# Performance work log

Measured on AMD Instinct MI355X. Metric: run time of the kernel, lower is better.

## Reference

```python
import jax, jax.numpy as jnp
import numpy as np

B, L, D = 4, 2048, 256
DI, DS, DCONV, DTR, K = 512, 16, 4, 16, 3  # d_inner, d_state, mamba conv, dt_rank, outer conv kernel
PAD = 1 * (K - 1)  # dilation*(kernel_size-1)
ALPHA = 0.5


def setup_inputs() -> dict:
    key = jax.random.key(0)
    ks = jax.random.split(key, 14)
    s = lambda k, shape, scale: jax.random.normal(k, shape, dtype=jnp.float32) * scale
    inp = {
        "x": s(ks[0], (B, L, D), 1.0),
        "ln_w": jnp.ones((D,), jnp.float32),
        "ln_b": jnp.zeros((D,), jnp.float32),
        "conv_w": s(ks[1], (D, D, K), 0.05),          # outer Conv1d weight (out,in,k)
        "conv_b": s(ks[2], (D,), 0.02),
        "in_proj_w": s(ks[3], (2 * DI, D), 0.05),      # Mamba in_proj (no bias)
        "conv1d_w": s(ks[4], (DI, 1, DCONV), 0.3),     # depthwise causal conv
        "conv1d_b": s(ks[5], (DI,), 0.02),
        "x_proj_w": s(ks[6], (DTR + 2 * DS, DI), 0.05),
        "dt_proj_w": s(ks[7], (DI, DTR), 0.1),
        "dt_proj_b": s(ks[8], (DI,), 0.1),
        "A_log": jnp.log(jnp.broadcast_to(jnp.arange(1, DS + 1, dtype=jnp.float32), (DI, DS))),
        "D_param": jnp.ones((DI,), jnp.float32),
        "out_proj_w": s(ks[9], (D, DI), 0.05),
    }
    return inp


def _layernorm(h, w, b):
    mu = jnp.mean(h, axis=-1, keepdims=True)
    var = jnp.mean(jnp.square(h - mu), axis=-1, keepdims=True)
    return (h - mu) * jax.lax.rsqrt(var + 1e-5) * w + b


def _causal_conv(h_ncl, w, pad, groups):
    # h_ncl: (B, C, L); left-pad only -> output length L (matches pad-then-slice in torch)
    return jax.lax.conv_general_dilated(
        h_ncl, w, window_strides=(1,), padding=[(pad, 0)],
        dimension_numbers=("NCH", "OIH", "NCH"), feature_group_count=groups)


def _mamba(h, in_proj_w, conv1d_w, conv1d_b, x_proj_w, dt_proj_w, dt_proj_b, A_log, D_param, out_proj_w):
    xz = jnp.einsum("bld,ed->ble", h, in_proj_w)          # (B,L,2*DI)
    xin, z = jnp.split(xz, 2, axis=-1)
    xc = _causal_conv(xin.transpose(0, 2, 1), conv1d_w, DCONV - 1, DI)
    xc = jax.nn.silu(xc + conv1d_b[None, :, None]).transpose(0, 2, 1)   # (B,L,DI)
    x_dbl = jnp.einsum("bld,ed->ble", xc, x_proj_w)
    dt, Bm, Cm = jnp.split(x_dbl, [DTR, DTR + DS], axis=-1)
    delta = jax.nn.softplus(jnp.einsum("blr,dr->bld", dt, dt_proj_w) + dt_proj_b)  # (B,L,DI)
    A = -jnp.exp(A_log)                                     # (DI,DS)
    dA = jnp.exp(delta[..., None] * A)                      # (B,L,DI,DS)
    dBx = delta[..., None] * Bm[:, :, None, :] * xc[..., None]

    def step(hst, t):
        dA_t, dBx_t, C_t = t
        hst = dA_t * hst + dBx_t                            # (B,DI,DS)
        y = jnp.einsum("bds,bs->bd", hst, C_t)
        return hst, y

    h0 = jnp.zeros((h.shape[0], DI, DS), h.dtype)
    _, ys = jax.lax.scan(step, h0, (dA.transpose(1, 0, 2, 3), dBx.transpose(1, 0, 2, 3), Cm.transpose(1, 0, 2)))
    y = ys.transpose(1, 0, 2) + xc * D_param                # (B,L,DI)
    y = y * jax.nn.silu(z)
    return jnp.einsum("ble,de->bld", y, out_proj_w)


def reference(x, ln_w, ln_b, conv_w, conv_b, in_proj_w, conv1d_w, conv1d_b,
              x_proj_w, dt_proj_w, dt_proj_b, A_log, D_param, out_proj_w):
    h = _layernorm(x, ln_w, ln_b)
    # conv branch: pad left, conv, GELU (exact erf, as torch nn.GELU)
    hc = _causal_conv(h.transpose(0, 2, 1), conv_w, PAD, 1) + conv_b[None, :, None]
    h_conv = jax.nn.gelu(hc, approximate=False).transpose(0, 2, 1)
    h_mamba = _mamba(h, in_proj_w, conv1d_w, conv1d_b, x_proj_w, dt_proj_w,
                     dt_proj_b, A_log, D_param, out_proj_w)
    h_out = ALPHA * h_mamba + (1.0 - ALPHA) * h_conv
    return x + h_out
```

## Files before the change

kernel.cpp:

```cpp
#include <hip/hip_runtime.h>
#include <math.h>

#define BBATCH 4
#define LSEQ   2048
#define DMODEL 256
#define DINNER 512
#define DSTATE 16
#define DTRANK 16
#define MROWS  (BBATCH * LSEQ)
#define NCHUNK 64
#define LCHUNK (LSEQ / NCHUNK)

typedef unsigned short u16;
typedef __attribute__((ext_vector_type(8))) short bf16x8;
typedef __attribute__((ext_vector_type(4))) float f32x4;

#define OFF_HBF    ((size_t)0)
#define OFF_HCONV  ((size_t)1048576)
#define OFF_XIN    ((size_t)3145728)
#define OFF_Z      ((size_t)7340032)
#define OFF_XC     ((size_t)11534336)
#define OFF_DELTA  ((size_t)15728640)
#define OFF_XDBL   ((size_t)19922944)
#define OFF_YBF    ((size_t)20316160)
#define OFF_AAGG   ((size_t)22413312)
#define OFF_BAGG   ((size_t)24510464)
#define OFF_HINIT  OFF_AAGG
#define OFF_WTINBF ((size_t)26607616)
#define OFF_WTCVBF ((size_t)26738688)
#define OFF_WTOUTBF ((size_t)26836992)
#define OFF_WTX    ((size_t)26902528)
#define OFF_WTDT   ((size_t)26927104)

__device__ __forceinline__ float silu_f(float v) {
  return v / (1.0f + __expf(-v));
}
__device__ __forceinline__ u16 f2bf(float f) {
  unsigned u = __float_as_uint(f);
  return (u16)((u + 0x7FFFu + ((u >> 16) & 1u)) >> 16);
}
__device__ __forceinline__ float bf2f(u16 v) {
  return __uint_as_float(((unsigned)v) << 16);
}

__global__ __launch_bounds__(256) void k_repack(
    const float* __restrict__ inw, const float* __restrict__ convw,
    const float* __restrict__ xw, const float* __restrict__ dtw,
    const float* __restrict__ ow, float* __restrict__ ws) {
  int idx = blockIdx.x * 256 + threadIdx.x;
  u16* win  = (u16*)(ws + OFF_WTINBF);
  u16* wcv  = (u16*)(ws + OFF_WTCVBF);
  u16* wout = (u16*)(ws + OFF_WTOUTBF);
  float* wx  = ws + OFF_WTX;
  float* wdt = ws + OFF_WTDT;
  if (idx < 262144) {
    win[idx] = f2bf(inw[idx]);
    return;
  }
  int i2 = idx - 262144;
  if (i2 < 196608) {
    int o = i2 / 768, r = i2 - o * 768;
    int kk = r >> 8, i = r & 255;
    wcv[i2] = f2bf(convw[(o * 256 + i) * 3 + kk]);
    return;
  }
  int i3 = i2 - 196608;
  if (i3 < 131072) {
    wout[i3] = f2bf(ow[i3]);
    return;
  }
  int i4 = i3 - 131072;
  if (i4 < 24576) {
    int k = i4 / 48, n = i4 - k * 48;
    wx[i4] = xw[n * 512 + k];
    return;
  }
  int i5 = i4 - 24576;
  if (i5 < 8192) {
    int r = i5 >> 9, n = i5 & 511;
    wdt[i5] = dtw[n * 16 + r];
  }
}

__global__ __launch_bounds__(256) void k_layernorm(
    const float* __restrict__ x, const float* __restrict__ w,
    const float* __restrict__ b, u16* __restrict__ hb) {
  int wave = threadIdx.x >> 6;
  int lane = threadIdx.x & 63;
  int row  = blockIdx.x * 4 + wave;
  const float4* xr = reinterpret_cast<const float4*>(x + (size_t)row * 256);
  float4 v = xr[lane];
  float s  = v.x + v.y + v.z + v.w;
  float sq = v.x*v.x + v.y*v.y + v.z*v.z + v.w*v.w;
  #pragma unroll
  for (int o = 32; o >= 1; o >>= 1) { s += __shfl_xor(s, o); sq += __shfl_xor(sq, o); }
  float mu  = s * (1.0f / 256.0f);
  float var = sq * (1.0f / 256.0f) - mu * mu;
  float rs  = rsqrtf(var + 1e-5f);
  float4 wv = reinterpret_cast<const float4*>(w)[lane];
  float4 bv = reinterpret_cast<const float4*>(b)[lane];
  ushort4 o4;
  o4.x = f2bf((v.x - mu) * rs * wv.x + bv.x);
  o4.y = f2bf((v.y - mu) * rs * wv.y + bv.y);
  o4.z = f2bf((v.z - mu) * rs * wv.z + bv.z);
  o4.w = f2bf((v.w - mu) * rs * wv.w + bv.w);
  reinterpret_cast<ushort4*>(hb + (size_t)row * 256)[lane] = o4;
}


__global__ __launch_bounds__(256) void k_bgemm_inproj(
    const u16* __restrict__ Abf, const u16* __restrict__ Bbf,
    u16* __restrict__ xin, u16* __restrict__ z) {
  __shared__ __align__(16) u16 As[64 * 72];
  __shared__ __align__(16) u16 Bs[128 * 72];
  int tid = threadIdx.x;
  int m0 = blockIdx.x * 64, n0 = blockIdx.y * 128;
  int lane = tid & 63, wid = tid >> 6;
  int wc = wid * 32;
  int l15 = lane & 15, lk = (lane >> 4) * 8;
  int r0 = tid >> 3, kc = (tid & 7) * 8;
  f32x4 acc[4][2] = {};
  for (int k0 = 0; k0 < 256; k0 += 64) {
    *(bf16x8*)&As[r0 * 72 + kc] =
        *(const bf16x8*)&Abf[(size_t)(m0 + r0) * 256 + k0 + kc];
    *(bf16x8*)&As[(r0 + 32) * 72 + kc] =
        *(const bf16x8*)&Abf[(size_t)(m0 + r0 + 32) * 256 + k0 + kc];
    #pragma unroll
    for (int rr = 0; rr < 4; ++rr)
      *(bf16x8*)&Bs[(r0 + rr * 32) * 72 + kc] =
          *(const bf16x8*)&Bbf[(size_t)(n0 + r0 + rr * 32) * 256 + k0 + kc];
    __syncthreads();
    #pragma unroll
    for (int kk = 0; kk < 64; kk += 32) {
      bf16x8 b0 = *(const bf16x8*)&Bs[(wc + l15) * 72 + kk + lk];
      bf16x8 b1 = *(const bf16x8*)&Bs[(wc + 16 + l15) * 72 + kk + lk];
      #pragma unroll
      for (int q = 0; q < 4; ++q) {
        bf16x8 a = *(const bf16x8*)&As[(q * 16 + l15) * 72 + kk + lk];
        acc[q][0] = __builtin_amdgcn_mfma_f32_16x16x32_bf16(a, b0, acc[q][0], 0, 0, 0);
        acc[q][1] = __builtin_amdgcn_mfma_f32_16x16x32_bf16(a, b1, acc[q][1], 0, 0, 0);
      }
    }
    __syncthreads();
  }
  u16* dst = (blockIdx.y < 4) ? xin : z;
  int nb = n0 & 511;
  int rsub = (lane >> 4) * 4;
  #pragma unroll
  for (int q = 0; q < 4; ++q)
    #pragma unroll
    for (int ni = 0; ni < 2; ++ni) {
      int gc = nb + wc + ni * 16 + l15;
      #pragma unroll
      for (int r = 0; r < 4; ++r)
        dst[(size_t)(m0 + q * 16 + rsub + r) * 512 + gc] = f2bf(acc[q][ni][r]);
    }
}

__global__ __launch_bounds__(256) void k_bgemm_conv(
    const u16* __restrict__ hbf, const u16* __restrict__ Bbf,
    const float* __restrict__ cb, float* __restrict__ hconv) {
  __shared__ __align__(16) u16 As[64 * 72];
  __shared__ __align__(16) u16 Bs[64 * 72];
  int tid = threadIdx.x;
  int m0 = blockIdx.x * 64, n0 = blockIdx.y * 64;
  int bidx = m0 >> 11, t0 = m0 & 2047;
  int lane = tid & 63, wid = tid >> 6;
  int wr = (wid >> 1) * 32, wc = (wid & 1) * 32;
  int l15 = lane & 15, lk = (lane >> 4) * 8;
  int r0 = tid >> 3, kc = (tid & 7) * 8;
  f32x4 acc[2][2] = {};
  for (int k0 = 0; k0 < 768; k0 += 64) {
    int kkc = k0 >> 8;
    int i0  = (k0 & 255) + kc;
    int t1  = t0 + r0 - 2 + kkc;
    bf16x8 av0 = {0, 0, 0, 0, 0, 0, 0, 0};
    if (t1 >= 0)
      av0 = *(const bf16x8*)&hbf[(size_t)((bidx << 11) + t1) * 256 + i0];
    bf16x8 av1 =
        *(const bf16x8*)&hbf[(size_t)((bidx << 11) + t1 + 32) * 256 + i0];
    *(bf16x8*)&As[r0 * 72 + kc] = av0;
    *(bf16x8*)&As[(r0 + 32) * 72 + kc] = av1;
    *(bf16x8*)&Bs[r0 * 72 + kc] =
        *(const bf16x8*)&Bbf[(size_t)(n0 + r0) * 768 + k0 + kc];
    *(bf16x8*)&Bs[(r0 + 32) * 72 + kc] =
        *(const bf16x8*)&Bbf[(size_t)(n0 + r0 + 32) * 768 + k0 + kc];
    __syncthreads();
    #pragma unroll
    for (int kk = 0; kk < 64; kk += 32) {
      bf16x8 a0 = *(const bf16x8*)&As[(wr + l15) * 72 + kk + lk];
      bf16x8 a1 = *(const bf16x8*)&As[(wr + 16 + l15) * 72 + kk + lk];
      bf16x8 b0 = *(const bf16x8*)&Bs[(wc + l15) * 72 + kk + lk];
      bf16x8 b1 = *(const bf16x8*)&Bs[(wc + 16 + l15) * 72 + kk + lk];
      acc[0][0] = __builtin_amdgcn_mfma_f32_16x16x32_bf16(a0, b0, acc[0][0], 0, 0, 0);
      acc[0][1] = __builtin_amdgcn_mfma_f32_16x16x32_bf16(a0, b1, acc[0][1], 0, 0, 0);
      acc[1][0] = __builtin_amdgcn_mfma_f32_16x16x32_bf16(a1, b0, acc[1][0], 0, 0, 0);
      acc[1][1] = __builtin_amdgcn_mfma_f32_16x16x32_bf16(a1, b1, acc[1][1], 0, 0, 0);
    }
    __syncthreads();
  }
  int rowb = m0 + wr + (lane >> 4) * 4;
  #pragma unroll
  for (int mi = 0; mi < 2; ++mi)
    #pragma unroll
    for (int ni = 0; ni < 2; ++ni) {
      int gc = n0 + wc + ni * 16 + l15;
      float bias = cb[gc];
      #pragma unroll
      for (int r = 0; r < 4; ++r) {
        float v = acc[mi][ni][r] + bias;
        float g = 0.5f * v * (1.0f + erff(v * 0.70710678118654752440f));
        hconv[(size_t)(rowb + mi * 16 + r) * 256 + gc] = g;
      }
    }
}

__global__ __launch_bounds__(256) void k_bgemm_outproj(
    const u16* __restrict__ Abf, const u16* __restrict__ Bbf,
    const float* __restrict__ x, const float* __restrict__ hconv,
    float* __restrict__ out) {
  __shared__ __align__(16) u16 As[64 * 72];
  __shared__ __align__(16) u16 Bs[64 * 72];
  int tid = threadIdx.x;
  int m0 = blockIdx.x * 64, n0 = blockIdx.y * 64;
  int lane = tid & 63, wid = tid >> 6;
  int wr = (wid >> 1) * 32, wc = (wid & 1) * 32;
  int l15 = lane & 15, lk = (lane >> 4) * 8;
  int r0 = tid >> 3, kc = (tid & 7) * 8;
  f32x4 acc[2][2] = {};
  for (int k0 = 0; k0 < 512; k0 += 64) {
    *(bf16x8*)&As[r0 * 72 + kc] =
        *(const bf16x8*)&Abf[(size_t)(m0 + r0) * 512 + k0 + kc];
    *(bf16x8*)&As[(r0 + 32) * 72 + kc] =
        *(const bf16x8*)&Abf[(size_t)(m0 + r0 + 32) * 512 + k0 + kc];
    *(bf16x8*)&Bs[r0 * 72 + kc] =
        *(const bf16x8*)&Bbf[(size_t)(n0 + r0) * 512 + k0 + kc];
    *(bf16x8*)&Bs[(r0 + 32) * 72 + kc] =
        *(const bf16x8*)&Bbf[(size_t)(n0 + r0 + 32) * 512 + k0 + kc];
    __syncthreads();
    #pragma unroll
    for (int kk = 0; kk < 64; kk += 32) {
      bf16x8 a0 = *(const bf16x8*)&As[(wr + l15) * 72 + kk + lk];
      bf16x8 a1 = *(const bf16x8*)&As[(wr + 16 + l15) * 72 + kk + lk];
      bf16x8 b0 = *(const bf16x8*)&Bs[(wc + l15) * 72 + kk + lk];
      bf16x8 b1 = *(const bf16x8*)&Bs[(wc + 16 + l15) * 72 + kk + lk];
      acc[0][0] = __builtin_amdgcn_mfma_f32_16x16x32_bf16(a0, b0, acc[0][0], 0, 0, 0);
      acc[0][1] = __builtin_amdgcn_mfma_f32_16x16x32_bf16(a0, b1, acc[0][1], 0, 0, 0);
      acc[1][0] = __builtin_amdgcn_mfma_f32_16x16x32_bf16(a1, b0, acc[1][0], 0, 0, 0);
      acc[1][1] = __builtin_amdgcn_mfma_f32_16x16x32_bf16(a1, b1, acc[1][1], 0, 0, 0);
    }
    __syncthreads();
  }
  int rowb = m0 + wr + (lane >> 4) * 4;
  #pragma unroll
  for (int mi = 0; mi < 2; ++mi)
    #pragma unroll
    for (int ni = 0; ni < 2; ++ni) {
      int gc = n0 + wc + ni * 16 + l15;
      #pragma unroll
      for (int r = 0; r < 4; ++r) {
        size_t off = (size_t)(rowb + mi * 16 + r) * 256 + gc;
        out[off] = x[off] + 0.5f * acc[mi][ni][r] + 0.5f * hconv[off];
      }
    }
}

__global__ __launch_bounds__(256) void k_gemm_xproj(
    const float* __restrict__ A, const float* __restrict__ Bt,
    float* __restrict__ C) {
  __shared__ float As[16][68];
  __shared__ float Bs[16][68];
  int tid = threadIdx.x;
  int m0 = blockIdx.x * 64;
  int ar = tid >> 2, ac = (tid & 3) * 4;
  int br = tid >> 4, bc = (tid & 15) * 4;
  int tx = tid & 15, ty = tid >> 4;
  float acc[4][4] = {};
  for (int k0 = 0; k0 < 512; k0 += 16) {
    float4 av = *reinterpret_cast<const float4*>(A + (size_t)(m0 + ar) * 512 + k0 + ac);
    As[ac + 0][ar] = av.x; As[ac + 1][ar] = av.y;
    As[ac + 2][ar] = av.z; As[ac + 3][ar] = av.w;
    float4 bv = make_float4(0.f, 0.f, 0.f, 0.f);
    if (bc < 48)
      bv = *reinterpret_cast<const float4*>(Bt + (size_t)(k0 + br) * 48 + bc);
    *reinterpret_cast<float4*>(&Bs[br][bc]) = bv;
    __syncthreads();
    #pragma unroll
    for (int kt = 0; kt < 16; ++kt) {
      float4 a = *reinterpret_cast<const float4*>(&As[kt][ty * 4]);
      float4 b = *reinterpret_cast<const float4*>(&Bs[kt][tx * 4]);
      acc[0][0]+=a.x*b.x; acc[0][1]+=a.x*b.y; acc[0][2]+=a.x*b.z; acc[0][3]+=a.x*b.w;
      acc[1][0]+=a.y*b.x; acc[1][1]+=a.y*b.y; acc[1][2]+=a.y*b.z; acc[1][3]+=a.y*b.w;
      acc[2][0]+=a.z*b.x; acc[2][1]+=a.z*b.y; acc[2][2]+=a.z*b.z; acc[2][3]+=a.z*b.w;
      acc[3][0]+=a.w*b.x; acc[3][1]+=a.w*b.y; acc[3][2]+=a.w*b.z; acc[3][3]+=a.w*b.w;
    }
    __syncthreads();
  }
  if (tx < 12) {
    #pragma unroll
    for (int i = 0; i < 4; ++i) {
      float4 cv = make_float4(acc[i][0], acc[i][1], acc[i][2], acc[i][3]);
      *reinterpret_cast<float4*>(C + (size_t)(m0 + ty * 4 + i) * 48 + tx * 4) = cv;
    }
  }
}

__global__ __launch_bounds__(256) void k_dtproj(
    const float* __restrict__ xdbl, const float* __restrict__ Wdt,
    const float* __restrict__ db, float* __restrict__ delta) {
  int m = blockIdx.x;
  __shared__ float dts[16];
  if (threadIdx.x < 16) dts[threadIdx.x] = xdbl[(size_t)m * 48 + threadIdx.x];
  __syncthreads();
  for (int di = threadIdx.x; di < 512; di += 256) {
    float acc = db[di];
    #pragma unroll
    for (int r = 0; r < 16; ++r) acc += dts[r] * Wdt[r * 512 + di];
    delta[(size_t)m * 512 + di] = (acc > 20.0f) ? acc : log1pf(__expf(acc));
  }
}

__global__ __launch_bounds__(256) void k_dwconv(
    const u16* __restrict__ xin, const float* __restrict__ cw,
    const float* __restrict__ cb, float* __restrict__ xc) {
  int idx = blockIdx.x * 256 + threadIdx.x;
  int di = idx & 511;
  int m  = idx >> 9;
  int t  = m & 2047;
  float w0 = cw[di * 4 + 0], w1 = cw[di * 4 + 1];
  float w2 = cw[di * 4 + 2], w3 = cw[di * 4 + 3];
  const u16* base = xin + (size_t)m * 512 + di;
  float acc = cb[di] + w3 * bf2f(base[0]);
  if (t >= 1) acc += w2 * bf2f(base[-512]);
  if (t >= 2) acc += w1 * bf2f(base[-1024]);
  if (t >= 3) acc += w0 * bf2f(base[-1536]);
  xc[(size_t)m * 512 + di] = silu_f(acc);
}

__global__ __launch_bounds__(256) void k_scan1(
    const float* __restrict__ delta, const float* __restrict__ xdbl,
    const float* __restrict__ xc, const float* __restrict__ Alog,
    float* __restrict__ Aagg, float* __restrict__ Bagg) {
  int di = ((blockIdx.x & 1) << 8) | threadIdx.x;
  int c  = (blockIdx.x >> 1) & 63;
  int b  = blockIdx.x >> 7;
  float nA[16];
  #pragma unroll
  for (int q = 0; q < 4; ++q) {
    float4 v = *reinterpret_cast<const float4*>(Alog + (size_t)di * 16 + q * 4);
    nA[q*4+0] = -__expf(v.x); nA[q*4+1] = -__expf(v.y);
    nA[q*4+2] = -__expf(v.z); nA[q*4+3] = -__expf(v.w);
  }
  float ap[16], bacc[16];
  #pragma unroll
  for (int s = 0; s < 16; ++s) { ap[s] = 1.0f; bacc[s] = 0.0f; }
  int row0 = b * 2048 + c * LCHUNK;
  const float* dp = delta + (size_t)row0 * 512 + di;
  const float* xp = xc    + (size_t)row0 * 512 + di;
  const float* Bp = xdbl  + (size_t)row0 * 48 + 16;
  #pragma unroll 2
  for (int t = 0; t < LCHUNK; ++t) {
    float dv = dp[t * 512];
    float u  = dv * xp[t * 512];
    #pragma unroll
    for (int s = 0; s < 16; ++s) {
      float e = __expf(dv * nA[s]);
      ap[s]   *= e;
      bacc[s]  = e * bacc[s] + u * Bp[t * 48 + s];
    }
  }
  size_t base = ((size_t)((b * 64 + c) * 16)) * 512 + di;
  #pragma unroll
  for (int s = 0; s < 16; ++s) {
    Aagg[base + (size_t)s * 512] = ap[s];
    Bagg[base + (size_t)s * 512] = bacc[s];
  }
}

__global__ __launch_bounds__(256) void k_scan2(
    const float* __restrict__ Aagg, const float* __restrict__ Bagg,
    float* __restrict__ Hinit) {
  int g  = blockIdx.x * 256 + threadIdx.x;
  int di = g & 511, s = (g >> 9) & 15, b = g >> 13;
  float h = 0.0f;
  for (int c = 0; c < NCHUNK; ++c) {
    size_t idx = ((size_t)((b * 64 + c) * 16 + s)) * 512 + di;
    float a = Aagg[idx], bb = Bagg[idx];
    Hinit[idx] = h;
    h = a * h + bb;
  }
}

__global__ __launch_bounds__(256) void k_scan3(
    const float* __restrict__ delta, const float* __restrict__ xdbl,
    const float* __restrict__ xc, const u16* __restrict__ z,
    const float* __restrict__ Alog, const float* __restrict__ Dp,
    const float* __restrict__ Hinit, u16* __restrict__ y) {
  int di = ((blockIdx.x & 1) << 8) | threadIdx.x;
  int c  = (blockIdx.x >> 1) & 63;
  int b  = blockIdx.x >> 7;
  float nA[16];
  #pragma unroll
  for (int q = 0; q < 4; ++q) {
    float4 v = *reinterpret_cast<const float4*>(Alog + (size_t)di * 16 + q * 4);
    nA[q*4+0] = -__expf(v.x); nA[q*4+1] = -__expf(v.y);
    nA[q*4+2] = -__expf(v.z); nA[q*4+3] = -__expf(v.w);
  }
  float h[16];
  size_t hb = ((size_t)((b * 64 + c) * 16)) * 512 + di;
  #pragma unroll
  for (int s = 0; s < 16; ++s) h[s] = Hinit[hb + (size_t)s * 512];
  float Dv = Dp[di];
  int row0 = b * 2048 + c * LCHUNK;
  const float* dp = delta + (size_t)row0 * 512 + di;
  const float* xp = xc    + (size_t)row0 * 512 + di;
  const u16*   zp = z     + (size_t)row0 * 512 + di;
  const float* Bp = xdbl  + (size_t)row0 * 48 + 16;
  const float* Cp = xdbl  + (size_t)row0 * 48 + 32;
  u16* yp         = y     + (size_t)row0 * 512 + di;
  #pragma unroll 2
  for (int t = 0; t < LCHUNK; ++t) {
    float dv  = dp[t * 512];
    float xcv = xp[t * 512];
    float u   = dv * xcv;
    float yv  = 0.0f;
    #pragma unroll
    for (int s = 0; s < 16; ++s) {
      float e = __expf(dv * nA[s]);
      h[s] = e * h[s] + u * Bp[t * 48 + s];
      yv  += h[s] * Cp[t * 48 + s];
    }
    yv += xcv * Dv;
    float zv = bf2f(zp[t * 512]);
    yp[t * 512] = f2bf(yv * silu_f(zv));
  }
}

extern "C" void kernel_launch(void* const* d_in, const int* in_sizes, int n_in,
                              void* d_out, int out_size, void* d_ws, size_t ws_size,
                              hipStream_t stream) {
  const float* x     = (const float*)d_in[0];
  const float* lnw   = (const float*)d_in[1];
  const float* lnb   = (const float*)d_in[2];
  const float* convw = (const float*)d_in[3];
  const float* convb = (const float*)d_in[4];
  const float* inw   = (const float*)d_in[5];
  const float* c1w   = (const float*)d_in[6];
  const float* c1b   = (const float*)d_in[7];
  const float* xw    = (const float*)d_in[8];
  const float* dtw   = (const float*)d_in[9];
  const float* dtb   = (const float*)d_in[10];
  const float* alog  = (const float*)d_in[11];
  const float* Dp    = (const float*)d_in[12];
  const float* ow    = (const float*)d_in[13];
  float* ws  = (float*)d_ws;
  float* out = (float*)d_out;

  u16* hbf     = (u16*)(ws + OFF_HBF);
  float* hconv = ws + OFF_HCONV;
  u16* xinbf   = (u16*)(ws + OFF_XIN);
  u16* zbf     = (u16*)(ws + OFF_Z);
  float* xc    = ws + OFF_XC;
  float* delta = ws + OFF_DELTA;
  float* xdbl  = ws + OFF_XDBL;
  u16* ybf     = (u16*)(ws + OFF_YBF);
  float* Aagg  = ws + OFF_AAGG;
  float* Bagg  = ws + OFF_BAGG;
  float* Hinit = ws + OFF_HINIT;
  u16* winbf   = (u16*)(ws + OFF_WTINBF);
  u16* wcvbf   = (u16*)(ws + OFF_WTCVBF);
  u16* woutbf  = (u16*)(ws + OFF_WTOUTBF);
  float* Wtx   = ws + OFF_WTX;
  float* Wtdt  = ws + OFF_WTDT;

  k_repack<<<2432, 256, 0, stream>>>(inw, convw, xw, dtw, ow, ws);
  k_layernorm<<<2048, 256, 0, stream>>>(x, lnw, lnb, hbf);
  k_bgemm_conv<<<dim3(128, 4), 256, 0, stream>>>(hbf, wcvbf, convb, hconv);
  k_bgemm_inproj<<<dim3(128, 8), 256, 0, stream>>>(hbf, winbf, xinbf, zbf);
  k_dwconv<<<16384, 256, 0, stream>>>(xinbf, c1w, c1b, xc);
  k_gemm_xproj<<<dim3(128, 1), 256, 0, stream>>>(xc, Wtx, xdbl);
  k_dtproj<<<8192, 256, 0, stream>>>(xdbl, Wtdt, dtb, delta);
  k_scan1<<<512, 256, 0, stream>>>(delta, xdbl, xc, alog, Aagg, Bagg);
  k_scan2<<<128, 256, 0, stream>>>(Aagg, Bagg, Hinit);
  k_scan3<<<512, 256, 0, stream>>>(delta, xdbl, xc, zbf, alog, Dp, Hinit, ybf);
  k_bgemm_outproj<<<dim3(128, 4), 256, 0, stream>>>(ybf, woutbf, x, hconv, out);
}
```

Before: 257.9 us.

## Retile x_proj GEMM for more blocks and batch rows in dt_proj

The x_proj GEMM moves from 128 blocks of 64 rows to 512 blocks of 16 rows. Each thread now computes three outputs, which raises parallelism on a GPU with many CUs, since 128 blocks underfilled the device. dt_proj now handles 32 rows per block and keeps the dt_proj weights in registers, instead of one row per block that reloaded weights from global memory each time. The cost is less register reuse in xproj, scalar rather than float4 global loads, and more register pressure in dtproj.

```diff
diff --git a/kernel.cpp b/kernel.cpp
--- a/kernel.cpp
+++ b/kernel.cpp
@@ -268,55 +268,66 @@
 __global__ __launch_bounds__(256) void k_gemm_xproj(
     const float* __restrict__ A, const float* __restrict__ Bt,
     float* __restrict__ C) {
-  __shared__ float As[16][68];
-  __shared__ float Bs[16][68];
+  __shared__ float As[16][17];
+  __shared__ float Bs[16][52];
   int tid = threadIdx.x;
-  int m0 = blockIdx.x * 64;
-  int ar = tid >> 2, ac = (tid & 3) * 4;
-  int br = tid >> 4, bc = (tid & 15) * 4;
-  int tx = tid & 15, ty = tid >> 4;
-  float acc[4][4] = {};
+  int m0 = blockIdx.x * 16;
+  int rr = tid >> 4, cg = tid & 15;
+  float acc0 = 0.f, acc1 = 0.f, acc2 = 0.f;
   for (int k0 = 0; k0 < 512; k0 += 16) {
-    float4 av = *reinterpret_cast<const float4*>(A + (size_t)(m0 + ar) * 512 + k0 + ac);
-    As[ac + 0][ar] = av.x; As[ac + 1][ar] = av.y;
-    As[ac + 2][ar] = av.z; As[ac + 3][ar] = av.w;
-    float4 bv = make_float4(0.f, 0.f, 0.f, 0.f);
-    if (bc < 48)
-      bv = *reinterpret_cast<const float4*>(Bt + (size_t)(k0 + br) * 48 + bc);
-    *reinterpret_cast<float4*>(&Bs[br][bc]) = bv;
+    As[rr][cg] = A[(size_t)(m0 + rr) * 512 + k0 + cg];
+    int e0 = tid;
+    Bs[e0 / 48][e0 % 48] = Bt[(size_t)(k0 + e0 / 48) * 48 + (e0 % 48)];
+    int e1 = tid + 256;
+    Bs[e1 / 48][e1 % 48] = Bt[(size_t)(k0 + e1 / 48) * 48 + (e1 % 48)];
+    int e2 = tid + 512;
+    if (e2 < 768)
+      Bs[e2 / 48][e2 % 48] = Bt[(size_t)(k0 + e2 / 48) * 48 + (e2 % 48)];
     __syncthreads();
     #pragma unroll
     for (int kt = 0; kt < 16; ++kt) {
-      float4 a = *reinterpret_cast<const float4*>(&As[kt][ty * 4]);
-      float4 b = *reinterpret_cast<const float4*>(&Bs[kt][tx * 4]);
-      acc[0][0]+=a.x*b.x; acc[0][1]+=a.x*b.y; acc[0][2]+=a.x*b.z; acc[0][3]+=a.x*b.w;
-      acc[1][0]+=a.y*b.x; acc[1][1]+=a.y*b.y; acc[1][2]+=a.y*b.z; acc[1][3]+=a.y*b.w;
-      acc[2][0]+=a.z*b.x; acc[2][1]+=a.z*b.y; acc[2][2]+=a.z*b.z; acc[2][3]+=a.z*b.w;
-      acc[3][0]+=a.w*b.x; acc[3][1]+=a.w*b.y; acc[3][2]+=a.w*b.z; acc[3][3]+=a.w*b.w;
-    }
-    __syncthreads();
-  }
-  if (tx < 12) {
-    #pragma unroll
-    for (int i = 0; i < 4; ++i) {
-      float4 cv = make_float4(acc[i][0], acc[i][1], acc[i][2], acc[i][3]);
-      *reinterpret_cast<float4*>(C + (size_t)(m0 + ty * 4 + i) * 48 + tx * 4) = cv;
-    }
-  }
+      float a = As[rr][kt];
+      acc0 += a * Bs[kt][cg * 3 + 0];
+      acc1 += a * Bs[kt][cg * 3 + 1];
+      acc2 += a * Bs[kt][cg * 3 + 2];
+    }
+    __syncthreads();
+  }
+  size_t o = (size_t)(m0 + rr) * 48 + cg * 3;
+  C[o + 0] = acc0;
+  C[o + 1] = acc1;
+  C[o + 2] = acc2;
 }
 
 __global__ __launch_bounds__(256) void k_dtproj(
     const float* __restrict__ xdbl, const float* __restrict__ Wdt,
     const float* __restrict__ db, float* __restrict__ delta) {
-  int m = blockIdx.x;
-  __shared__ float dts[16];
-  if (threadIdx.x < 16) dts[threadIdx.x] = xdbl[(size_t)m * 48 + threadIdx.x];
+  __shared__ float dts[32][17];
+  int tid = threadIdx.x;
+  int m0 = blockIdx.x * 32;
+  {
+    int rr = tid >> 4, cc = tid & 15;
+    dts[rr][cc]      = xdbl[(size_t)(m0 + rr) * 48 + cc];
+    dts[rr + 16][cc] = xdbl[(size_t)(m0 + rr + 16) * 48 + cc];
+  }
   __syncthreads();
-  for (int di = threadIdx.x; di < 512; di += 256) {
-    float acc = db[di];
-    #pragma unroll
-    for (int r = 0; r < 16; ++r) acc += dts[r] * Wdt[r * 512 + di];
-    delta[(size_t)m * 512 + di] = (acc > 20.0f) ? acc : log1pf(__expf(acc));
+  float wv0[16], wv1[16];
+  #pragma unroll
+  for (int r = 0; r < 16; ++r) {
+    wv0[r] = Wdt[r * 512 + tid];
+    wv1[r] = Wdt[r * 512 + tid + 256];
+  }
+  float b0 = db[tid], b1 = db[tid + 256];
+  for (int m = 0; m < 32; ++m) {
+    float a0 = b0, a1 = b1;
+    #pragma unroll
+    for (int r = 0; r < 16; ++r) {
+      float d = dts[m][r];
+      a0 += d * wv0[r];
+      a1 += d * wv1[r];
+    }
+    delta[(size_t)(m0 + m) * 512 + tid]       = (a0 > 20.0f) ? a0 : log1pf(__expf(a0));
+    delta[(size_t)(m0 + m) * 512 + tid + 256] = (a1 > 20.0f) ? a1 : log1pf(__expf(a1));
   }
 }
 
@@ -478,8 +489,8 @@
   k_bgemm_conv<<<dim3(128, 4), 256, 0, stream>>>(hbf, wcvbf, convb, hconv);
   k_bgemm_inproj<<<dim3(128, 8), 256, 0, stream>>>(hbf, winbf, xinbf, zbf);
   k_dwconv<<<16384, 256, 0, stream>>>(xinbf, c1w, c1b, xc);
-  k_gemm_xproj<<<dim3(128, 1), 256, 0, stream>>>(xc, Wtx, xdbl);
-  k_dtproj<<<8192, 256, 0, stream>>>(xdbl, Wtdt, dtb, delta);
+  k_gemm_xproj<<<512, 256, 0, stream>>>(xc, Wtx, xdbl);
+  k_dtproj<<<256, 256, 0, stream>>>(xdbl, Wtdt, dtb, delta);
   k_scan1<<<512, 256, 0, stream>>>(delta, xdbl, xc, alog, Aagg, Bagg);
   k_scan2<<<128, 256, 0, stream>>>(Aagg, Bagg, Hinit);
   k_scan3<<<512, 256, 0, stream>>>(delta, xdbl, xc, zbf, alog, Dp, Hinit, ybf);
```

After: 365.4 us. 41.7% more time.
